# Optimization experiments

Hardware: AMD Instinct MI355X
Metric: run time of the kernel (lower is better)

Reference implementation:

```python
import jax, jax.numpy as jnp
import numpy as np

LEAKY_SLOPE = 0.01  # torch F.leaky_relu default

N_NODES = 100000
N_EDGES = 1600000
IN_CH, HID_CH, OUT_CH = 128, 64, 32


def glorot(key, shape):
    fan_in, fan_out = shape
    lim = jnp.sqrt(6.0 / (fan_in + fan_out))
    return jax.random.uniform(key, shape, jnp.float32, -lim, lim)


def setup_inputs() -> dict:
    key = jax.random.key(0)
    ks = jax.random.split(key, 10)
    x = jax.random.normal(ks[0], (N_NODES, IN_CH), jnp.float32)
    edge_index = jax.random.randint(ks[1], (2, N_EDGES), 0, N_NODES, jnp.int64)
    return {
        "x": x,
        "edge_index": edge_index,
        "W1": glorot(ks[2], (IN_CH, HID_CH)),
        "b1": jnp.zeros((HID_CH,), jnp.float32),
        "W2": glorot(ks[3], (HID_CH, HID_CH)),
        "b2": jnp.zeros((HID_CH,), jnp.float32),
        "W_mu": glorot(ks[4], (HID_CH, OUT_CH)),
        "b_mu": jnp.zeros((OUT_CH,), jnp.float32),
        "W_ls": glorot(ks[5], (HID_CH, OUT_CH)),
        "b_ls": jnp.zeros((OUT_CH,), jnp.float32),
    }


def _gcn_norm(edge_index, n_nodes):
    """Symmetric GCN normalization with self-loops (PyG GCNConv default)."""
    src, dst = edge_index[0], edge_index[1]
    ones = jnp.ones((src.shape[0],), jnp.float32)
    deg = jax.ops.segment_sum(ones, dst, num_segments=n_nodes) + 1.0  # +1 self-loop
    dis = jax.lax.rsqrt(deg)  # deg >= 1 so no div-by-zero
    edge_w = dis[src] * dis[dst]          # [E] normalization per edge
    self_w = dis * dis                    # [N] self-loop normalization
    return src, dst, edge_w, self_w


def _gcn_conv(h, W, b, src, dst, edge_w, self_w, n_nodes):
    h = h @ W                                           # [N, C_out]
    msg = h[src] * edge_w[:, None]                      # gather + scale, [E, C_out]
    agg = jax.ops.segment_sum(msg, dst, num_segments=n_nodes)
    agg = agg + h * self_w[:, None]                     # self-loop term
    return agg + b


def reference(x, edge_index, W1, b1, W2, b2, W_mu, b_mu, W_ls, b_ls):
    n = x.shape[0]
    src, dst, ew, sw = _gcn_norm(edge_index, n)
    # dropout is identity in eval mode (reference baseline)
    h = jax.nn.leaky_relu(_gcn_conv(x, W1, b1, src, dst, ew, sw, n), LEAKY_SLOPE)
    h = jax.nn.leaky_relu(_gcn_conv(h, W2, b2, src, dst, ew, sw, n), LEAKY_SLOPE)
    mu = _gcn_conv(h, W_mu, b_mu, src, dst, ew, sw, n)
    logstd = _gcn_conv(h, W_ls, b_ls, src, dst, ew, sw, n)
    return mu, logstd
```

## Files before the change

kernel.cpp:

```cpp
#include <hip/hip_runtime.h>

#define LEAKY_SLOPE 0.01f
#define CBSH 7
#define CBSZ 128
#define CHUNK 4096

__device__ __forceinline__ unsigned short f2bf(float f) {
    unsigned int u = __builtin_bit_cast(unsigned int, f);
    u = (u + 0x7FFFu + ((u >> 16) & 1u)) >> 16;
    return (unsigned short)u;
}
__device__ __forceinline__ float bf2f(unsigned short h) {
    return __builtin_bit_cast(float, ((unsigned int)h) << 16);
}
__device__ __forceinline__ float ulof(unsigned u) {
    return __builtin_bit_cast(float, u << 16);
}
__device__ __forceinline__ float uhif(unsigned u) {
    return __builtin_bit_cast(float, u & 0xFFFF0000u);
}

__global__ __launch_bounds__(256) void chist_kernel(const int* __restrict__ dst,
                                                    int* __restrict__ cbin, int E, int ncb) {
    __shared__ int bins[1024];
    for (int i = threadIdx.x; i < 1024; i += 256) bins[i] = 0;
    __syncthreads();
    int stride = gridDim.x * blockDim.x;
    for (int e = blockIdx.x * blockDim.x + threadIdx.x; e < E; e += stride)
        atomicAdd(&bins[dst[e] >> CBSH], 1);
    __syncthreads();
    for (int i = threadIdx.x; i < ncb; i += 256) {
        int v = bins[i];
        if (v) atomicAdd(&cbin[i], v);
    }
}

__global__ __launch_bounds__(256) void cscan_kernel(const int* __restrict__ cbin,
                                                    int* __restrict__ cboff,
                                                    int* __restrict__ ccur16, int ncb) {
    __shared__ int s[256];
    __shared__ int carry;
    int t = threadIdx.x;
    if (t == 0) carry = 0;
    __syncthreads();
    for (int base = 0; base < ncb; base += 256) {
        int v = (base + t < ncb) ? cbin[base + t] : 0;
        s[t] = v;
        __syncthreads();
        for (int off = 1; off < 256; off <<= 1) {
            int u = (t >= off) ? s[t - off] : 0;
            __syncthreads();
            s[t] += u;
            __syncthreads();
        }
        int excl = carry + s[t] - v;
        if (base + t < ncb) { cboff[base + t] = excl; ccur16[(size_t)(base + t) * 16] = excl; }
        __syncthreads();
        if (t == 0) carry += s[255];
        __syncthreads();
    }
    if (t == 0) cboff[ncb] = carry;
}

__global__ __launch_bounds__(256) void scat1_kernel(const int* __restrict__ src,
                                                    const int* __restrict__ dst,
                                                    int* __restrict__ ccur16,
                                                    unsigned* __restrict__ pairs, int E) {
    __shared__ int bins[1024];
    __shared__ int base[1024];
    int t = threadIdx.x;
    for (int i = t; i < 1024; i += 256) bins[i] = 0;
    __syncthreads();
    int e0 = blockIdx.x * CHUNK;
    int m = min(CHUNK, E - e0);
    for (int i = t; i < m; i += 256)
        atomicAdd(&bins[dst[e0 + i] >> CBSH], 1);
    __syncthreads();
    for (int i = t; i < 1024; i += 256) {
        int c = bins[i];
        base[i] = c ? atomicAdd(&ccur16[(size_t)i * 16], c) : 0;
        bins[i] = 0;
    }
    __syncthreads();
    for (int i = t; i < m; i += 256) {
        int d = dst[e0 + i];
        int b = d >> CBSH;
        int off = atomicAdd(&bins[b], 1);
        pairs[base[b] + off] = (unsigned)src[e0 + i] | ((unsigned)(d & (CBSZ - 1)) << 17);
    }
}

__global__ __launch_bounds__(256) void degbuild_kernel(const unsigned* __restrict__ pairs,
                                                       const int* __restrict__ cboff,
                                                       float* __restrict__ dis,
                                                       int* __restrict__ dpad, int n) {
    __shared__ int cnt[CBSZ];
    int t = threadIdx.x;
    int b = blockIdx.x;
    if (t < CBSZ) cnt[t] = 0;
    __syncthreads();
    int e1 = cboff[b + 1];
    for (int e = cboff[b] + t; e < e1; e += 256)
        atomicAdd(&cnt[pairs[e] >> 17], 1);
    __syncthreads();
    if (t < CBSZ) {
        int node = b * CBSZ + t;
        if (node < n) {
            int d = cnt[t];
            dis[node] = rsqrtf((float)d + 1.0f);
            dpad[node] = (d + 15) & ~15;
        }
    }
}

__global__ void scan_block_sums(const int* __restrict__ deg, int* __restrict__ bsum, int n) {
    __shared__ int sdata[256];
    int i = blockIdx.x * 256 + threadIdx.x;
    int t = threadIdx.x;
    sdata[t] = (i < n) ? deg[i] : 0;
    __syncthreads();
    for (int s = 128; s > 0; s >>= 1) {
        if (t < s) sdata[t] += sdata[t + s];
        __syncthreads();
    }
    if (t == 0) bsum[blockIdx.x] = sdata[0];
}

__global__ void scan_partials(int* __restrict__ bsum, int nb, int* __restrict__ rp_end) {
    __shared__ int s[512];
    int t = threadIdx.x;
    int orig = (t < nb) ? bsum[t] : 0;
    s[t] = orig;
    __syncthreads();
    for (int off = 1; off < 512; off <<= 1) {
        int v = (t >= off) ? s[t - off] : 0;
        __syncthreads();
        s[t] += v;
        __syncthreads();
    }
    if (t < nb) bsum[t] = s[t] - orig;
    if (t == 0) rp_end[0] = s[511];
}

__global__ void scan_final(const int* __restrict__ deg, const int* __restrict__ bsum,
                           int* __restrict__ rp, int n) {
    __shared__ int s[256];
    int i = blockIdx.x * 256 + threadIdx.x;
    int t = threadIdx.x;
    int orig = (i < n) ? deg[i] : 0;
    s[t] = orig;
    __syncthreads();
    for (int off = 1; off < 256; off <<= 1) {
        int v = (t >= off) ? s[t - off] : 0;
        __syncthreads();
        s[t] += v;
        __syncthreads();
    }
    if (i < n) rp[i] = s[t] - orig + bsum[blockIdx.x];
}

__global__ void prefill_kernel(int* __restrict__ ssrc, int val, int total) {
    int i = blockIdx.x * blockDim.x + threadIdx.x;
    if (i < total) ssrc[i] = val;
}

__global__ __launch_bounds__(256) void scat2_kernel(const unsigned* __restrict__ pairs,
                                                    const int* __restrict__ cboff,
                                                    const int* __restrict__ rp,
                                                    int* __restrict__ ssrc, int n) {
    __shared__ int lrp[CBSZ];
    __shared__ int lcnt[CBSZ];
    int t = threadIdx.x;
    int b = blockIdx.x;
    if (t < CBSZ) {
        int node = b * CBSZ + t;
        lrp[t] = (node < n) ? rp[node] : 0;
        lcnt[t] = 0;
    }
    __syncthreads();
    int e1 = cboff[b + 1];
    for (int e = cboff[b] + t; e < e1; e += 256) {
        unsigned p = pairs[e];
        int dl = p >> 17;
        int off = atomicAdd(&lcnt[dl], 1);
        ssrc[lrp[dl] + off] = (int)(p & 0x1FFFFu);
    }
}

__global__ __launch_bounds__(256) void gemm1_kernel(const float* __restrict__ X,
                                                    const float* __restrict__ W,
                                                    const float* __restrict__ dis,
                                                    unsigned short* __restrict__ Hh, int N) {
    __shared__ float Xs[16 * 128];
    int tid = threadIdx.x;
    int row0 = blockIdx.x * 16;
    for (int i = tid * 4; i < 16 * 128; i += 256 * 4)
        *(float4*)&Xs[i] = *(const float4*)&X[(size_t)row0 * 128 + i];
    __syncthreads();

    int c = tid & 63;
    int g = tid >> 6;
    float acc[4] = {0.f, 0.f, 0.f, 0.f};
    for (int kk = 0; kk < 128; kk += 16) {
        float w[16];
#pragma unroll
        for (int k = 0; k < 16; ++k) w[k] = W[(kk + k) * 64 + c];
#pragma unroll
        for (int r = 0; r < 4; ++r) {
            int row = g + r * 4;
#pragma unroll
            for (int k4 = 0; k4 < 16; k4 += 4) {
                float4 x4 = *(float4*)&Xs[row * 128 + kk + k4];
                acc[r] += x4.x * w[k4] + x4.y * w[k4 + 1] + x4.z * w[k4 + 2] + x4.w * w[k4 + 3];
            }
        }
    }
#pragma unroll
    for (int r = 0; r < 4; ++r) {
        int row = row0 + g + r * 4;
        Hh[(size_t)row * 64 + c] = f2bf(acc[r] * dis[row]);
    }
}

#define GATHER_WIDE(Hh, wid, lane, accv)                                       \
    float accv;                                                                \
    {                                                                          \
        int gg = (lane) >> 4, cc = (lane) & 15;                                \
        float ac0 = 0.f, ac1 = 0.f, ac2 = 0.f, ac3 = 0.f;                      \
        int e0 = rp[wid], e1 = rp[(wid) + 1];                                  \
        const int* sp = ssrc + e0;                                             \
        int cnt = e1 - e0;                                                     \
        for (int i = 0; i < cnt; i += 16) {                                    \
            int s0 = sp[i + gg];                                               \
            int s1 = sp[i + gg + 4];                                           \
            int s2 = sp[i + gg + 8];                                           \
            int s3 = sp[i + gg + 12];                                          \
            uint2 q0 = *(const uint2*)&Hh[(size_t)s0 * 64 + cc * 4];           \
            uint2 q1 = *(const uint2*)&Hh[(size_t)s1 * 64 + cc * 4];           \
            uint2 q2 = *(const uint2*)&Hh[(size_t)s2 * 64 + cc * 4];           \
            uint2 q3 = *(const uint2*)&Hh[(size_t)s3 * 64 + cc * 4];           \
            ac0 += (ulof(q0.x) + ulof(q1.x)) + (ulof(q2.x) + ulof(q3.x));      \
            ac1 += (uhif(q0.x) + uhif(q1.x)) + (uhif(q2.x) + uhif(q3.x));      \
            ac2 += (ulof(q0.y) + ulof(q1.y)) + (ulof(q2.y) + ulof(q3.y));      \
            ac3 += (uhif(q0.y) + uhif(q1.y)) + (uhif(q2.y) + uhif(q3.y));      \
        }                                                                      \
        ac0 += __shfl_xor(ac0, 16); ac0 += __shfl_xor(ac0, 32);                \
        ac1 += __shfl_xor(ac1, 16); ac1 += __shfl_xor(ac1, 32);                \
        ac2 += __shfl_xor(ac2, 16); ac2 += __shfl_xor(ac2, 32);                \
        ac3 += __shfl_xor(ac3, 16); ac3 += __shfl_xor(ac3, 32);                \
        int srcl = (lane) >> 2;                                                \
        float v0 = __shfl(ac0, srcl);                                          \
        float v1 = __shfl(ac1, srcl);                                          \
        float v2 = __shfl(ac2, srcl);                                          \
        float v3 = __shfl(ac3, srcl);                                          \
        int jj = (lane) & 3;                                                   \
        accv = jj == 0 ? v0 : (jj == 1 ? v1 : (jj == 2 ? v2 : v3));            \
        accv += bf2f(Hh[(size_t)(wid) * 64 + (lane)]);                         \
    }

__global__ __launch_bounds__(256) void aggA_kernel(
    const unsigned short* __restrict__ Hh, const int* __restrict__ rp,
    const int* __restrict__ ssrc, const float* __restrict__ dis,
    const float* __restrict__ b1, const float* __restrict__ W2,
    unsigned short* __restrict__ Oh, int n) {
    int lane = threadIdx.x & 63;
    float wc[64];
#pragma unroll
    for (int k = 0; k < 64; ++k) wc[k] = W2[k * 64 + lane];
    float bias = b1[lane];

    int wid = (int)((blockIdx.x * blockDim.x + threadIdx.x) >> 6);
    int nwaves = (int)((gridDim.x * blockDim.x) >> 6);
    for (; wid < n; wid += nwaves) {
        GATHER_WIDE(Hh, wid, lane, accv)
        float d = dis[wid];
        float h = fmaf(accv, d, bias);
        h = h > 0.f ? h : LEAKY_SLOPE * h;
        int hb = __builtin_bit_cast(int, h);
        float o = 0.f;
#pragma unroll
        for (int k = 0; k < 64; ++k) {
            float hk = __builtin_bit_cast(float, __builtin_amdgcn_readlane(hb, k));
            o = fmaf(hk, wc[k], o);
        }
        Oh[(size_t)wid * 64 + lane] = f2bf(o * d);
    }
}

__global__ __launch_bounds__(256) void aggB_kernel(
    const unsigned short* __restrict__ Hh, const int* __restrict__ rp,
    const int* __restrict__ ssrc, const float* __restrict__ dis,
    const float* __restrict__ b2, unsigned short* __restrict__ Oh, int n) {
    int lane = threadIdx.x & 63;
    float bias = b2[lane];
    int wid = (int)((blockIdx.x * blockDim.x + threadIdx.x) >> 6);
    int nwaves = (int)((gridDim.x * blockDim.x) >> 6);
    for (; wid < n; wid += nwaves) {
        GATHER_WIDE(Hh, wid, lane, accv)
        float d = dis[wid];
        float h = fmaf(accv, d, bias);
        h = h > 0.f ? h : LEAKY_SLOPE * h;
        Oh[(size_t)wid * 64 + lane] = f2bf(h * d);
    }
}

__global__ __launch_bounds__(256) void aggC_kernel(
    const unsigned short* __restrict__ Hh, const int* __restrict__ rp,
    const int* __restrict__ ssrc, const float* __restrict__ dis,
    const float* __restrict__ Wmu, const float* __restrict__ bmu,
    const float* __restrict__ Wls, const float* __restrict__ bls,
    float* __restrict__ mu, float* __restrict__ ls, int n) {
    int lane = threadIdx.x & 63;
    int half = lane >> 5;
    int c = lane & 31;
    const float* Wp = half ? Wls : Wmu;
    float wc[64];
#pragma unroll
    for (int k = 0; k < 64; ++k) wc[k] = Wp[k * 32 + c];
    float bias = half ? bls[c] : bmu[c];
    float* outp = half ? ls : mu;

    int wid = (int)((blockIdx.x * blockDim.x + threadIdx.x) >> 6);
    int nwaves = (int)((gridDim.x * blockDim.x) >> 6);
    for (; wid < n; wid += nwaves) {
        GATHER_WIDE(Hh, wid, lane, accv)
        float gval = accv * dis[wid];
        int gb = __builtin_bit_cast(int, gval);
        float o = bias;
#pragma unroll
        for (int k = 0; k < 64; ++k) {
            float gk = __builtin_bit_cast(float, __builtin_amdgcn_readlane(gb, k));
            o = fmaf(gk, wc[k], o);
        }
        outp[(size_t)wid * 32 + c] = o;
    }
}

extern "C" void kernel_launch(void* const* d_in, const int* in_sizes, int n_in,
                              void* d_out, int out_size, void* d_ws, size_t ws_size,
                              hipStream_t stream) {
    const float* x   = (const float*)d_in[0];
    const int*   ei  = (const int*)d_in[1];
    const float* W1  = (const float*)d_in[2];
    const float* b1  = (const float*)d_in[3];
    const float* W2  = (const float*)d_in[4];
    const float* b2  = (const float*)d_in[5];
    const float* Wmu = (const float*)d_in[6];
    const float* bmu = (const float*)d_in[7];
    const float* Wls = (const float*)d_in[8];
    const float* bls = (const float*)d_in[9];

    const int N = in_sizes[0] / 128;
    const int E = in_sizes[1] / 2;
    const int NCB = (N + CBSZ - 1) / CBSZ;
    const int PADMAX = E + 15 * ((N + 15) / 16) * 16 + 64;
    const int* src  = ei;
    const int* dstp = ei + E;

    auto align64 = [](size_t v) { return (v + 63) & ~(size_t)63; };
    char* ws = (char*)d_ws;
    int*   dpad   = (int*)ws;   ws += align64((size_t)N * 4);
    float* dis    = (float*)ws; ws += align64((size_t)N * 4);
    int*   cbin   = (int*)ws;   ws += align64(1024 * 4);
    int*   cboff  = (int*)ws;   ws += align64(1025 * 4);
    int*   ccur16 = (int*)ws;   ws += align64((size_t)1024 * 16 * 4);
    int*   bsum   = (int*)ws;   ws += 4096;
    int*   rp     = (int*)ws;   ws += align64((size_t)(N + 1) * 4);
    unsigned* pairs = (unsigned*)ws; ws += align64((size_t)E * 4);
    int*   ssrc   = (int*)ws;   ws += align64((size_t)PADMAX * 4);
    unsigned short* bufH0 = (unsigned short*)ws; ws += align64(((size_t)N + 1) * 64 * 2);
    unsigned short* bufH1 = (unsigned short*)ws; ws += align64(((size_t)N + 1) * 64 * 2);

    float* mu = (float*)d_out;
    float* ls = mu + (size_t)N * 32;

    const int nblocks = (N + 255) / 256;
    const int s1blocks = (E + CHUNK - 1) / CHUNK;

    hipMemsetAsync(cbin, 0, 1024 * sizeof(int), stream);
    prefill_kernel<<<(PADMAX + 255) / 256, 256, 0, stream>>>(ssrc, N, PADMAX);
    chist_kernel<<<256, 256, 0, stream>>>(dstp, cbin, E, NCB);
    cscan_kernel<<<1, 256, 0, stream>>>(cbin, cboff, ccur16, NCB);
    scat1_kernel<<<s1blocks, 256, 0, stream>>>(src, dstp, ccur16, pairs, E);
    degbuild_kernel<<<NCB, 256, 0, stream>>>(pairs, cboff, dis, dpad, N);
    scan_block_sums<<<nblocks, 256, 0, stream>>>(dpad, bsum, N);
    scan_partials<<<1, 512, 0, stream>>>(bsum, nblocks, rp + N);
    scan_final<<<nblocks, 256, 0, stream>>>(dpad, bsum, rp, N);
    scat2_kernel<<<NCB, 256, 0, stream>>>(pairs, cboff, rp, ssrc, N);

    gemm1_kernel<<<N / 16, 256, 0, stream>>>(x, W1, dis, bufH0, N);
    hipMemsetAsync(bufH0 + (size_t)N * 64, 0, 128, stream);
    hipMemsetAsync(bufH1 + (size_t)N * 64, 0, 128, stream);

    const int aggblocks = 2048;

    aggA_kernel<<<aggblocks, 256, 0, stream>>>(bufH0, rp, ssrc, dis, b1, W2, bufH1, N);
    aggB_kernel<<<aggblocks, 256, 0, stream>>>(bufH1, rp, ssrc, dis, b2, bufH0, N);
    aggC_kernel<<<aggblocks, 256, 0, stream>>>(bufH0, rp, ssrc, dis, Wmu, bmu,
                                               Wls, bls, mu, ls, N);
}
```

Before: 307.4 us.

## Move matvec weights to LDS, vectorize index loads, pad adjacency in scatter

Moves the per-lane 64-register weight arrays in the aggregation kernels into shared memory and splits the matvec into four independent accumulators. The aim is lower register pressure and higher occupancy for the latency-bound gather. The gather now fetches four neighbor indices with a single int4 load, using a contiguous layout within each 16-entry group. The separate prefill kernel is removed, and scat2 now writes the dummy-node padding itself, saving a full-buffer write. The cost is an extra LDS read per FMA and a per-block weight load at kernel start.

```diff
diff --git a/kernel.cpp b/kernel.cpp
--- a/kernel.cpp
+++ b/kernel.cpp
@@ -18,6 +18,9 @@
 }
 __device__ __forceinline__ float uhif(unsigned u) {
     return __builtin_bit_cast(float, u & 0xFFFF0000u);
+}
+__device__ __forceinline__ float bcastf(int hb, int k) {
+    return __builtin_bit_cast(float, __builtin_amdgcn_readlane(hb, k));
 }
 
 __global__ __launch_bounds__(256) void chist_kernel(const int* __restrict__ dst,
@@ -159,11 +162,6 @@
     if (i < n) rp[i] = s[t] - orig + bsum[blockIdx.x];
 }
 
-__global__ void prefill_kernel(int* __restrict__ ssrc, int val, int total) {
-    int i = blockIdx.x * blockDim.x + threadIdx.x;
-    if (i < total) ssrc[i] = val;
-}
-
 __global__ __launch_bounds__(256) void scat2_kernel(const unsigned* __restrict__ pairs,
                                                     const int* __restrict__ cboff,
                                                     const int* __restrict__ rp,
@@ -184,6 +182,16 @@
         int dl = p >> 17;
         int off = atomicAdd(&lcnt[dl], 1);
         ssrc[lrp[dl] + off] = (int)(p & 0x1FFFFu);
+    }
+    __syncthreads();
+    if (t < CBSZ) {
+        int node = b * CBSZ + t;
+        if (node < n) {
+            int c0 = lcnt[t];
+            int cpad = (c0 + 15) & ~15;
+            int base = lrp[t];
+            for (int i = c0; i < cpad; ++i) ssrc[base + i] = n;
+        }
     }
 }
 
@@ -231,14 +239,11 @@
         const int* sp = ssrc + e0;                                             \
         int cnt = e1 - e0;                                                     \
         for (int i = 0; i < cnt; i += 16) {                                    \
-            int s0 = sp[i + gg];                                               \
-            int s1 = sp[i + gg + 4];                                           \
-            int s2 = sp[i + gg + 8];                                           \
-            int s3 = sp[i + gg + 12];                                          \
-            uint2 q0 = *(const uint2*)&Hh[(size_t)s0 * 64 + cc * 4];           \
-            uint2 q1 = *(const uint2*)&Hh[(size_t)s1 * 64 + cc * 4];           \
-            uint2 q2 = *(const uint2*)&Hh[(size_t)s2 * 64 + cc * 4];           \
-            uint2 q3 = *(const uint2*)&Hh[(size_t)s3 * 64 + cc * 4];           \
+            int4 s4 = *(const int4*)&sp[i + gg * 4];                           \
+            uint2 q0 = *(const uint2*)&Hh[(size_t)s4.x * 64 + cc * 4];         \
+            uint2 q1 = *(const uint2*)&Hh[(size_t)s4.y * 64 + cc * 4];         \
+            uint2 q2 = *(const uint2*)&Hh[(size_t)s4.z * 64 + cc * 4];         \
+            uint2 q3 = *(const uint2*)&Hh[(size_t)s4.w * 64 + cc * 4];         \
             ac0 += (ulof(q0.x) + ulof(q1.x)) + (ulof(q2.x) + ulof(q3.x));      \
             ac1 += (uhif(q0.x) + uhif(q1.x)) + (uhif(q2.x) + uhif(q3.x));      \
             ac2 += (ulof(q0.y) + ulof(q1.y)) + (ulof(q2.y) + ulof(q3.y));      \
@@ -258,15 +263,31 @@
         accv += bf2f(Hh[(size_t)(wid) * 64 + (lane)]);                         \
     }
 
+#define LDS_MATVEC(hb, lane, Ws, o)                                            \
+    float o;                                                                   \
+    {                                                                          \
+        float o0 = 0.f, o1 = 0.f, o2 = 0.f, o3 = 0.f;                          \
+        _Pragma("unroll")                                                      \
+        for (int k = 0; k < 64; k += 4) {                                      \
+            o0 = fmaf(bcastf(hb, k),     Ws[(k)*64 + (lane)],     o0);         \
+            o1 = fmaf(bcastf(hb, k + 1), Ws[(k+1)*64 + (lane)], o1);           \
+            o2 = fmaf(bcastf(hb, k + 2), Ws[(k+2)*64 + (lane)], o2);           \
+            o3 = fmaf(bcastf(hb, k + 3), Ws[(k+3)*64 + (lane)], o3);           \
+        }                                                                      \
+        o = (o0 + o1) + (o2 + o3);                                             \
+    }
+
 __global__ __launch_bounds__(256) void aggA_kernel(
     const unsigned short* __restrict__ Hh, const int* __restrict__ rp,
     const int* __restrict__ ssrc, const float* __restrict__ dis,
     const float* __restrict__ b1, const float* __restrict__ W2,
     unsigned short* __restrict__ Oh, int n) {
+    __shared__ float Ws[64 * 64];
+    for (int i = threadIdx.x * 4; i < 4096; i += 256 * 4)
+        *(float4*)&Ws[i] = *(const float4*)&W2[i];
+    __syncthreads();
+
     int lane = threadIdx.x & 63;
-    float wc[64];
-#pragma unroll
-    for (int k = 0; k < 64; ++k) wc[k] = W2[k * 64 + lane];
     float bias = b1[lane];
 
     int wid = (int)((blockIdx.x * blockDim.x + threadIdx.x) >> 6);
@@ -277,12 +298,7 @@
         float h = fmaf(accv, d, bias);
         h = h > 0.f ? h : LEAKY_SLOPE * h;
         int hb = __builtin_bit_cast(int, h);
-        float o = 0.f;
-#pragma unroll
-        for (int k = 0; k < 64; ++k) {
-            float hk = __builtin_bit_cast(float, __builtin_amdgcn_readlane(hb, k));
-            o = fmaf(hk, wc[k], o);
-        }
+        LDS_MATVEC(hb, lane, Ws, o)
         Oh[(size_t)wid * 64 + lane] = f2bf(o * d);
     }
 }
@@ -310,13 +326,16 @@
     const float* __restrict__ Wmu, const float* __restrict__ bmu,
     const float* __restrict__ Wls, const float* __restrict__ bls,
     float* __restrict__ mu, float* __restrict__ ls, int n) {
+    __shared__ float Ws[64 * 64];
+    for (int i = threadIdx.x; i < 4096; i += 256) {
+        int k = i >> 6, c = i & 63;
+        Ws[i] = (c < 32) ? Wmu[k * 32 + c] : Wls[k * 32 + (c - 32)];
+    }
+    __syncthreads();
+
     int lane = threadIdx.x & 63;
     int half = lane >> 5;
     int c = lane & 31;
-    const float* Wp = half ? Wls : Wmu;
-    float wc[64];
-#pragma unroll
-    for (int k = 0; k < 64; ++k) wc[k] = Wp[k * 32 + c];
     float bias = half ? bls[c] : bmu[c];
     float* outp = half ? ls : mu;
 
@@ -326,13 +345,8 @@
         GATHER_WIDE(Hh, wid, lane, accv)
         float gval = accv * dis[wid];
         int gb = __builtin_bit_cast(int, gval);
-        float o = bias;
-#pragma unroll
-        for (int k = 0; k < 64; ++k) {
-            float gk = __builtin_bit_cast(float, __builtin_amdgcn_readlane(gb, k));
-            o = fmaf(gk, wc[k], o);
-        }
-        outp[(size_t)wid * 32 + c] = o;
+        LDS_MATVEC(gb, lane, Ws, o)
+        outp[(size_t)wid * 32 + c] = o + bias;
     }
 }
 
@@ -378,7 +392,6 @@
     const int s1blocks = (E + CHUNK - 1) / CHUNK;
 
     hipMemsetAsync(cbin, 0, 1024 * sizeof(int), stream);
-    prefill_kernel<<<(PADMAX + 255) / 256, 256, 0, stream>>>(ssrc, N, PADMAX);
     chist_kernel<<<256, 256, 0, stream>>>(dstp, cbin, E, NCB);
     cscan_kernel<<<1, 256, 0, stream>>>(cbin, cboff, ccur16, NCB);
     scat1_kernel<<<s1blocks, 256, 0, stream>>>(src, dstp, ccur16, pairs, E);
```

New measurement: 305.3 us. About the same (-0.7%).
